# Kernel tuning notes

Measured on AMD Instinct MI355X. Metric: run time of the kernel, lower is better.

The kernel has to match this reference:

```python
import jax, jax.numpy as jnp
import numpy as np

E, K, H, I, T = 32, 4, 1024, 1024, 1024
ALPHA, BETA = 1.702, 1.0  # swiglu_alpha, swiglu_beta from the module


def setup_inputs() -> dict:
    key = jax.random.key(0)
    k0, k1, k2, k3 = jax.random.split(key, 4)
    return {
        "hidden_states": jax.random.normal(k0, (T, H), jnp.float32),
        "gate_w": jax.random.normal(k1, (H, E), jnp.float32) * (H ** -0.5),
        "gate_b": jnp.zeros((E,), jnp.float32),
        # pair_wise_act=True: gate/up are interleaved along the last dim of w1's output
        "w1": jax.random.normal(k2, (E, H, 2 * I), jnp.float32) * (H ** -0.5),
        "b1": jnp.zeros((E, 2 * I), jnp.float32),
        "w2": jax.random.normal(k3, (E, I, H), jnp.float32) * (I ** -0.5),
        "b2": jnp.zeros((E, H), jnp.float32),
    }


def reference(hidden_states, gate_w, gate_b, w1, b1, w2, b2):
    # Router gate (ReplicatedLinear with bias)
    router_logits = hidden_states @ gate_w + gate_b            # [T, E]
    probs = jax.nn.softmax(router_logits, axis=-1)
    topk_w, topk_idx = jax.lax.top_k(probs, K)                 # [T, K]
    # renormalize (norm_topk_prob=True)
    topk_w = topk_w / jnp.sum(topk_w, axis=-1, keepdims=True)
    # combine weights per (expert, token): sum over slots where idx == e
    onehot = (topk_idx[None, :, :] == jnp.arange(E)[:, None, None])  # [E, T, K]
    combine_w = jnp.sum(onehot * topk_w[None, :, :], axis=-1)        # [E, T]
    # Expert MLPs (grouped GEMM expressed as dense-per-expert einsum)
    h = jnp.einsum('th,ehd->etd', hidden_states, w1) + b1[:, None, :]  # [E, T, 2I]
    gate = h[..., 0::2]   # interleaved pairwise gate
    up = h[..., 1::2]     # interleaved pairwise up
    act = (up + BETA) * gate * jax.nn.sigmoid(ALPHA * gate)           # [E, T, I]
    y = jnp.einsum('eti,eih->eth', act, w2) + b2[:, None, :]          # [E, T, H]
    # weighted combine across selected experts
    return jnp.einsum('eth,et->th', y, combine_w)                     # [T, H]
```

## Files before the change

### kernel.cpp

```cpp
#include <hip/hip_runtime.h>
#include <hip/hip_bf16.h>
#include <math.h>

#define E_ 32
#define K_ 4
#define H_ 1024
#define I_ 1024
#define T_ 1024
#define TWO_I 2048

typedef __attribute__((ext_vector_type(4))) float float4v;
typedef __attribute__((ext_vector_type(8))) short short8v;
typedef __attribute__((ext_vector_type(4))) short short4v;

__device__ __forceinline__ unsigned short f2bf(float f) {
    unsigned u = __float_as_uint(f);
    u = (u + 0x7FFFu + ((u >> 16) & 1u)) >> 16;
    return (unsigned short)u;
}
__device__ __forceinline__ short4v cvt4(float4v v) {
    union { unsigned u[2]; short4v s; } r;
    asm("v_cvt_pk_bf16_f32 %0, %1, %2" : "=v"(r.u[0]) : "v"(v[0]), "v"(v[1]));
    asm("v_cvt_pk_bf16_f32 %0, %1, %2" : "=v"(r.u[1]) : "v"(v[2]), "v"(v[3]));
    return r.s;
}
__device__ __forceinline__ int permpos(int k4) {
    return ((k4 >> 5) << 5) + (((k4 >> 2) & 3) << 3) + (((k4 >> 4) & 1) << 2);
}

__global__ __launch_bounds__(256) void hs2bf_kernel(
    const float* __restrict__ hs, unsigned short* __restrict__ hsb) {
    int i = blockIdx.x * 256 + threadIdx.x;
    float4v v = *(const float4v*)(hs + (size_t)i * 4);
    *(short4v*)(hsb + (size_t)i * 4) = cvt4(v);
}

__global__ __launch_bounds__(256) void router_kernel(
    const float* __restrict__ hs, const float* __restrict__ gw,
    const float* __restrict__ gb, int* __restrict__ counts,
    int* __restrict__ token_list, float* __restrict__ weight_list) {
    int wv = threadIdx.x >> 6, lane = threadIdx.x & 63;
    int t = blockIdx.x * 4 + wv;
    int e = lane & 31;
    int half = lane >> 5;
    const float* hrow = hs + (size_t)t * H_;
    const float* gcol = gw + e;
    float a0 = 0.f, a1 = 0.f;
    int hb = half * 512;
#pragma unroll 4
    for (int h = 0; h < 512; h += 2) {
        a0 = fmaf(hrow[hb + h],     gcol[(size_t)(hb + h) * E_], a0);
        a1 = fmaf(hrow[hb + h + 1], gcol[(size_t)(hb + h + 1) * E_], a1);
    }
    float part = a0 + a1;
    part += __shfl_xor(part, 32);
    float cur = part + gb[e];

    int idx4[K_]; float val4[K_];
#pragma unroll
    for (int k = 0; k < K_; ++k) {
        float m = cur;
#pragma unroll
        for (int d = 1; d < 64; d <<= 1) m = fmaxf(m, __shfl_xor(m, d));
        unsigned long long b = __ballot(cur == m);
        int l = __ffsll(b) - 1;
        idx4[k] = l & 31; val4[k] = m;
        if (e == (l & 31)) cur = -INFINITY;
    }
    float mx = val4[0], s = 0.f, wv4[K_];
#pragma unroll
    for (int k = 0; k < K_; ++k) { wv4[k] = expf(val4[k] - mx); s += wv4[k]; }
    float inv = 1.f / s;
    if (lane < K_) {
        int ex = idx4[lane];
        int slot = atomicAdd(&counts[ex], 1);
        token_list[ex * T_ + slot] = t;
        weight_list[ex * T_ + slot] = wv4[lane] * inv;
    }
}

#define G_COMPUTE(BUF)                                                         \
    _Pragma("unroll")                                                          \
    for (int s = 0; s < 2; ++s) {                                              \
        short8v afr[4];                                                        \
        _Pragma("unroll")                                                      \
        for (int mi = 0; mi < 4; ++mi) {                                       \
            int row = wm * 64 + mi * 16 + l15;                                 \
            afr[mi] = *(const short8v*)&As[BUF][row * 64 + ((s * 32 + g * 8) ^ sw)]; \
        }                                                                      \
        short4v bl[2], bh[2];                                                  \
        _Pragma("unroll")                                                      \
        for (int ni = 0; ni < 2; ++ni) {                                       \
            unsigned ad = ((BUF) ? trb1 : trb0) + (unsigned)(ni * 2048 + s * 1024); \
            asm volatile("ds_read_b64_tr_b16 %0, %1" : "=v"(bl[ni]) : "v"(ad));     \
            asm volatile("ds_read_b64_tr_b16 %0, %1" : "=v"(bh[ni]) : "v"(ad + 512u)); \
        }                                                                      \
        asm volatile("s_waitcnt lgkmcnt(0)" ::: "memory");                     \
        __builtin_amdgcn_sched_barrier(0);                                     \
        _Pragma("unroll")                                                      \
        for (int ni = 0; ni < 2; ++ni) {                                       \
            short8v b;                                                         \
            b[0] = bl[ni][0]; b[1] = bl[ni][1]; b[2] = bl[ni][2]; b[3] = bl[ni][3]; \
            b[4] = bh[ni][0]; b[5] = bh[ni][1]; b[6] = bh[ni][2]; b[7] = bh[ni][3]; \
            _Pragma("unroll")                                                  \
            for (int mi = 0; mi < 4; ++mi)                                     \
                acc[mi][ni] = __builtin_amdgcn_mfma_f32_16x16x32_bf16(afr[mi], b, acc[mi][ni], 0, 0, 0); \
        }                                                                      \
    }

#define G_STEP(BUF, KN, BSTRIDE, ISLAST)                                       \
    {                                                                          \
        __syncthreads();                                                       \
        if (!(ISLAST)) {                                                       \
            _Pragma("unroll")                                                  \
            for (int i = 0; i < 4; ++i)                                        \
                ra[i] = aptr[i] ? *(const short8v*)(aptr[i] + (KN)) : z8;      \
            _Pragma("unroll")                                                  \
            for (int i = 0; i < 4; ++i)                                        \
                rb[i] = *(const float4v*)(bptrB + (size_t)(KN) * (BSTRIDE) + (size_t)(i * 16) * (BSTRIDE)); \
        }                                                                      \
        __builtin_amdgcn_sched_barrier(0);                                     \
        G_COMPUTE(BUF)                                                         \
        if (!(ISLAST)) {                                                       \
            _Pragma("unroll")                                                  \
            for (int i = 0; i < 4; ++i) {                                      \
                short8v v = ra[i];                                             \
                short4v lo, hi;                                                \
                lo[0] = v[0]; lo[1] = v[1]; lo[2] = v[2]; lo[3] = v[3];        \
                hi[0] = v[4]; hi[1] = v[5]; hi[2] = v[6]; hi[3] = v[7];        \
                *(short4v*)&As[(BUF) ^ 1][aw0[i]] = lo;                        \
                *(short4v*)&As[(BUF) ^ 1][aw1[i]] = hi;                        \
            }                                                                  \
            _Pragma("unroll")                                                  \
            for (int i = 0; i < 4; ++i) *(short4v*)&Bs[(BUF) ^ 1][bwidx[i]] = cvt4(rb[i]); \
        }                                                                      \
    }

__global__ __launch_bounds__(256, 3) void gemm1_kernel(
    const unsigned short* __restrict__ hsb, const float* __restrict__ w1,
    const float* __restrict__ b1, const int* __restrict__ counts,
    const int* __restrict__ token_list, unsigned short* __restrict__ actb) {
    int e = blockIdx.z;
    int cnt = counts[e];
    int m0 = blockIdx.y * 128;
    if (m0 >= cnt) return;
    int cb = blockIdx.x * 64;
    const float* w1e = w1 + (size_t)e * H_ * TWO_I;
    const int* tl = token_list + e * T_;

    __shared__ __align__(16) short As[2][128 * 64];
    __shared__ __align__(16) short Bs[2][64 * 64];

    int tid = threadIdx.x;
    int lane = tid & 63;
    int wid = tid >> 6;
    int wm = wid >> 1, wn = wid & 1;
    int g = lane >> 4;
    int l15 = lane & 15;
    int sw = (l15 & 7) << 3;
    unsigned trb0 = (unsigned)(size_t)(&Bs[0][0]) + (unsigned)(lane * 8) + (unsigned)(wn * 4096);
    unsigned trb1 = (unsigned)(size_t)(&Bs[1][0]) + (unsigned)(lane * 8) + (unsigned)(wn * 4096);

    int q = tid & 7;
    const unsigned short* aptr[4]; int aw0[4], aw1[4];
#pragma unroll
    for (int i = 0; i < 4; ++i) {
        int row = i * 32 + (tid >> 3);
        int gr = m0 + row;
        aptr[i] = (gr < cnt) ? hsb + (size_t)tl[gr] * H_ + q * 8 : nullptr;
        int swr = (row & 7) << 3;
        aw0[i] = row * 64 + (permpos(q * 8) ^ swr);
        aw1[i] = row * 64 + (permpos(q * 8 + 4) ^ swr);
    }
    int c4 = (tid & 15) << 2;
    const float* bptrB = w1e + (size_t)(tid >> 4) * TWO_I + cb + c4;
    int bwidx[4];
#pragma unroll
    for (int i = 0; i < 4; ++i) {
        int krow = i * 16 + (tid >> 4);
        bwidx[i] = ((c4 >> 4) * 16 + (krow >> 2)) * 64 + (krow & 3) * 16 + (c4 & 15);
    }

    float4v acc[4][2];
#pragma unroll
    for (int i = 0; i < 4; ++i)
#pragma unroll
        for (int j = 0; j < 2; ++j) acc[i][j] = (float4v){0.f, 0.f, 0.f, 0.f};

    short8v ra[4]; float4v rb[4];
    const short8v z8 = {0, 0, 0, 0, 0, 0, 0, 0};
#pragma unroll
    for (int i = 0; i < 4; ++i) ra[i] = aptr[i] ? *(const short8v*)(aptr[i]) : z8;
#pragma unroll
    for (int i = 0; i < 4; ++i) rb[i] = *(const float4v*)(bptrB + (size_t)(i * 16) * TWO_I);
#pragma unroll
    for (int i = 0; i < 4; ++i) {
        short8v v = ra[i];
        short4v lo, hi;
        lo[0] = v[0]; lo[1] = v[1]; lo[2] = v[2]; lo[3] = v[3];
        hi[0] = v[4]; hi[1] = v[5]; hi[2] = v[6]; hi[3] = v[7];
        *(short4v*)&As[0][aw0[i]] = lo;
        *(short4v*)&As[0][aw1[i]] = hi;
    }
#pragma unroll
    for (int i = 0; i < 4; ++i) *(short4v*)&Bs[0][bwidx[i]] = cvt4(rb[i]);

#pragma unroll 1
    for (int kk = 0; kk < H_; kk += 128) {
        G_STEP(0, kk + 64, TWO_I, false)
        G_STEP(1, kk + 128, TWO_I, (kk + 128) >= H_)
    }

    const float* b1e = b1 + (size_t)e * TWO_I;
#pragma unroll
    for (int mi = 0; mi < 4; ++mi) {
#pragma unroll
        for (int r = 0; r < 4; ++r) {
            int gm = m0 + wm * 64 + mi * 16 + g * 4 + r;
#pragma unroll
            for (int ni = 0; ni < 2; ++ni) {
                float v = acc[mi][ni][r];
                float o = __shfl_xor(v, 1);
                if (!(lane & 1) && gm < cnt) {
                    int wc = cb + wn * 32 + ni * 16 + l15;
                    float gate = v + b1e[wc];
                    float up   = o + b1e[wc + 1];
                    float sg = 1.f / (1.f + __expf(-1.702f * gate));
                    float av = (up + 1.f) * gate * sg;
                    actb[(size_t)(e * T_ + gm) * I_ + (wc >> 1)] = f2bf(av);
                }
            }
        }
    }
}

__global__ __launch_bounds__(256, 3) void gemm2_kernel(
    const unsigned short* __restrict__ actb, const float* __restrict__ w2,
    const float* __restrict__ b2, const int* __restrict__ counts,
    const int* __restrict__ token_list, const float* __restrict__ weight_list,
    float* __restrict__ out) {
    int e = blockIdx.z;
    int cnt = counts[e];
    int m0 = blockIdx.y * 128;
    if (m0 >= cnt) return;
    int h0 = (blockIdx.x >> 1) * 64;
    int kbase = (blockIdx.x & 1) * 512;
    const float* w2e = w2 + (size_t)e * I_ * H_;
    const int* tl = token_list + e * T_;

    __shared__ __align__(16) short As[2][128 * 64];
    __shared__ __align__(16) short Bs[2][64 * 64];

    int tid = threadIdx.x;
    int lane = tid & 63;
    int wid = tid >> 6;
    int wm = wid >> 1, wn = wid & 1;
    int g = lane >> 4;
    int l15 = lane & 15;
    int sw = (l15 & 7) << 3;
    unsigned trb0 = (unsigned)(size_t)(&Bs[0][0]) + (unsigned)(lane * 8) + (unsigned)(wn * 4096);
    unsigned trb1 = (unsigned)(size_t)(&Bs[1][0]) + (unsigned)(lane * 8) + (unsigned)(wn * 4096);

    int q = tid & 7;
    const unsigned short* aptr[4]; int aw0[4], aw1[4];
#pragma unroll
    for (int i = 0; i < 4; ++i) {
        int row = i * 32 + (tid >> 3);
        int gr = m0 + row;
        aptr[i] = (gr < cnt) ? actb + (size_t)(e * T_ + gr) * I_ + kbase + q * 8 : nullptr;
        int swr = (row & 7) << 3;
        aw0[i] = row * 64 + (permpos(q * 8) ^ swr);
        aw1[i] = row * 64 + (permpos(q * 8 + 4) ^ swr);
    }
    int c4 = (tid & 15) << 2;
    const float* bptrB = w2e + (size_t)(kbase + (tid >> 4)) * H_ + h0 + c4;
    int bwidx[4];
#pragma unroll
    for (int i = 0; i < 4; ++i) {
        int krow = i * 16 + (tid >> 4);
        bwidx[i] = ((c4 >> 4) * 16 + (krow >> 2)) * 64 + (krow & 3) * 16 + (c4 & 15);
    }

    float4v acc[4][2];
#pragma unroll
    for (int i = 0; i < 4; ++i)
#pragma unroll
        for (int j = 0; j < 2; ++j) acc[i][j] = (float4v){0.f, 0.f, 0.f, 0.f};

    short8v ra[4]; float4v rb[4];
    const short8v z8 = {0, 0, 0, 0, 0, 0, 0, 0};
#pragma unroll
    for (int i = 0; i < 4; ++i) ra[i] = aptr[i] ? *(const short8v*)(aptr[i]) : z8;
#pragma unroll
    for (int i = 0; i < 4; ++i) rb[i] = *(const float4v*)(bptrB + (size_t)(i * 16) * H_);
#pragma unroll
    for (int i = 0; i < 4; ++i) {
        short8v v = ra[i];
        short4v lo, hi;
        lo[0] = v[0]; lo[1] = v[1]; lo[2] = v[2]; lo[3] = v[3];
        hi[0] = v[4]; hi[1] = v[5]; hi[2] = v[6]; hi[3] = v[7];
        *(short4v*)&As[0][aw0[i]] = lo;
        *(short4v*)&As[0][aw1[i]] = hi;
    }
#pragma unroll
    for (int i = 0; i < 4; ++i) *(short4v*)&Bs[0][bwidx[i]] = cvt4(rb[i]);

#pragma unroll 1
    for (int kk = 0; kk < 512; kk += 128) {
        G_STEP(0, kk + 64, H_, false)
        G_STEP(1, kk + 128, H_, (kk + 128) >= 512)
    }

    const float* b2e = b2 + (size_t)e * H_;
    const float* wl = weight_list + e * T_;
    bool addbias = (kbase == 0);
#pragma unroll
    for (int mi = 0; mi < 4; ++mi) {
#pragma unroll
        for (int r = 0; r < 4; ++r) {
            int gm = m0 + wm * 64 + mi * 16 + g * 4 + r;
            if (gm < cnt) {
                int t = tl[gm];
                float wgt = wl[gm];
#pragma unroll
                for (int ni = 0; ni < 2; ++ni) {
                    int h = h0 + wn * 32 + ni * 16 + l15;
                    float v = acc[mi][ni][r];
                    if (addbias) v += b2e[h];
                    atomicAdd(&out[(size_t)t * H_ + h], v * wgt);
                }
            }
        }
    }
}

extern "C" void kernel_launch(void* const* d_in, const int* in_sizes, int n_in,
                              void* d_out, int out_size, void* d_ws, size_t ws_size,
                              hipStream_t stream) {
    const float* hs = (const float*)d_in[0];
    const float* gw = (const float*)d_in[1];
    const float* gb = (const float*)d_in[2];
    const float* w1 = (const float*)d_in[3];
    const float* b1 = (const float*)d_in[4];
    const float* w2 = (const float*)d_in[5];
    const float* b2 = (const float*)d_in[6];
    float* out = (float*)d_out;

    char* ws = (char*)d_ws;
    int*   counts      = (int*)ws;
    int*   token_list  = (int*)(ws + 4096);
    float* weight_list = (float*)(ws + 4096 + 131072);
    unsigned short* hsb  = (unsigned short*)(ws + (1 << 20));
    unsigned short* actb = (unsigned short*)(ws + (1 << 20) + (2 << 20));

    hipMemsetAsync(counts, 0, 32 * sizeof(int), stream);
    hipMemsetAsync(d_out, 0, (size_t)out_size * sizeof(float), stream);

    hs2bf_kernel<<<(T_ * H_ / 4) / 256, 256, 0, stream>>>(hs, hsb);
    router_kernel<<<T_ / 4, 256, 0, stream>>>(hs, gw, gb, counts, token_list, weight_list);
    gemm1_kernel<<<dim3(TWO_I / 64, T_ / 128, E_), 256, 0, stream>>>(
        hsb, w1, b1, counts, token_list, actb);
    gemm2_kernel<<<dim3((H_ / 64) * 2, T_ / 128, E_), 256, 0, stream>>>(
        actb, w2, b2, counts, token_list, weight_list, out);
}
```

Baseline: 203.9 us.

## Single-buffer A tile to fit four blocks per CU and fuse memsets into prep

The A operand shared-memory tile becomes single-buffered, with an extra barrier after compute before the next A tile is stored. This lowers LDS per block from 48KB to 32KB so launch bounds can rise to 4 blocks per CU. The two memsets (counts and output) move into the bf16 conversion kernel to save launches. The cost is an extra __syncthreads per k-step and less overlap between loading A and computing on it.

```diff
diff --git a/kernel.cpp b/kernel.cpp
--- a/kernel.cpp
+++ b/kernel.cpp
@@ -28,11 +28,14 @@
     return ((k4 >> 5) << 5) + (((k4 >> 2) & 3) << 3) + (((k4 >> 4) & 1) << 2);
 }
 
-__global__ __launch_bounds__(256) void hs2bf_kernel(
-    const float* __restrict__ hs, unsigned short* __restrict__ hsb) {
+__global__ __launch_bounds__(256) void prep_kernel(
+    const float* __restrict__ hs, unsigned short* __restrict__ hsb,
+    float* __restrict__ out, int* __restrict__ counts) {
     int i = blockIdx.x * 256 + threadIdx.x;
     float4v v = *(const float4v*)(hs + (size_t)i * 4);
     *(short4v*)(hsb + (size_t)i * 4) = cvt4(v);
+    *(float4v*)(out + (size_t)i * 4) = (float4v){0.f, 0.f, 0.f, 0.f};
+    if (blockIdx.x == 0 && threadIdx.x < E_) counts[threadIdx.x] = 0;
 }
 
 __global__ __launch_bounds__(256) void router_kernel(
@@ -86,7 +89,7 @@
         _Pragma("unroll")                                                      \
         for (int mi = 0; mi < 4; ++mi) {                                       \
             int row = wm * 64 + mi * 16 + l15;                                 \
-            afr[mi] = *(const short8v*)&As[BUF][row * 64 + ((s * 32 + g * 8) ^ sw)]; \
+            afr[mi] = *(const short8v*)&As[row * 64 + ((s * 32 + g * 8) ^ sw)]; \
         }                                                                      \
         short4v bl[2], bh[2];                                                  \
         _Pragma("unroll")                                                      \
@@ -121,6 +124,7 @@
         }                                                                      \
         __builtin_amdgcn_sched_barrier(0);                                     \
         G_COMPUTE(BUF)                                                         \
+        __syncthreads();                                                       \
         if (!(ISLAST)) {                                                       \
             _Pragma("unroll")                                                  \
             for (int i = 0; i < 4; ++i) {                                      \
@@ -128,15 +132,15 @@
                 short4v lo, hi;                                                \
                 lo[0] = v[0]; lo[1] = v[1]; lo[2] = v[2]; lo[3] = v[3];        \
                 hi[0] = v[4]; hi[1] = v[5]; hi[2] = v[6]; hi[3] = v[7];        \
-                *(short4v*)&As[(BUF) ^ 1][aw0[i]] = lo;                        \
-                *(short4v*)&As[(BUF) ^ 1][aw1[i]] = hi;                        \
+                *(short4v*)&As[aw0[i]] = lo;                                   \
+                *(short4v*)&As[aw1[i]] = hi;                                   \
             }                                                                  \
             _Pragma("unroll")                                                  \
             for (int i = 0; i < 4; ++i) *(short4v*)&Bs[(BUF) ^ 1][bwidx[i]] = cvt4(rb[i]); \
         }                                                                      \
     }
 
-__global__ __launch_bounds__(256, 3) void gemm1_kernel(
+__global__ __launch_bounds__(256, 4) void gemm1_kernel(
     const unsigned short* __restrict__ hsb, const float* __restrict__ w1,
     const float* __restrict__ b1, const int* __restrict__ counts,
     const int* __restrict__ token_list, unsigned short* __restrict__ actb) {
@@ -148,7 +152,7 @@
     const float* w1e = w1 + (size_t)e * H_ * TWO_I;
     const int* tl = token_list + e * T_;
 
-    __shared__ __align__(16) short As[2][128 * 64];
+    __shared__ __align__(16) short As[128 * 64];
     __shared__ __align__(16) short Bs[2][64 * 64];
 
     int tid = threadIdx.x;
@@ -199,8 +203,8 @@
         short4v lo, hi;
         lo[0] = v[0]; lo[1] = v[1]; lo[2] = v[2]; lo[3] = v[3];
         hi[0] = v[4]; hi[1] = v[5]; hi[2] = v[6]; hi[3] = v[7];
-        *(short4v*)&As[0][aw0[i]] = lo;
-        *(short4v*)&As[0][aw1[i]] = hi;
+        *(short4v*)&As[aw0[i]] = lo;
+        *(short4v*)&As[aw1[i]] = hi;
     }
 #pragma unroll
     for (int i = 0; i < 4; ++i) *(short4v*)&Bs[0][bwidx[i]] = cvt4(rb[i]);
@@ -234,7 +238,7 @@
     }
 }
 
-__global__ __launch_bounds__(256, 3) void gemm2_kernel(
+__global__ __launch_bounds__(256, 4) void gemm2_kernel(
     const unsigned short* __restrict__ actb, const float* __restrict__ w2,
     const float* __restrict__ b2, const int* __restrict__ counts,
     const int* __restrict__ token_list, const float* __restrict__ weight_list,
@@ -248,7 +252,7 @@
     const float* w2e = w2 + (size_t)e * I_ * H_;
     const int* tl = token_list + e * T_;
 
-    __shared__ __align__(16) short As[2][128 * 64];
+    __shared__ __align__(16) short As[128 * 64];
     __shared__ __align__(16) short Bs[2][64 * 64];
 
     int tid = threadIdx.x;
@@ -299,8 +303,8 @@
         short4v lo, hi;
         lo[0] = v[0]; lo[1] = v[1]; lo[2] = v[2]; lo[3] = v[3];
         hi[0] = v[4]; hi[1] = v[5]; hi[2] = v[6]; hi[3] = v[7];
-        *(short4v*)&As[0][aw0[i]] = lo;
-        *(short4v*)&As[0][aw1[i]] = hi;
+        *(short4v*)&As[aw0[i]] = lo;
+        *(short4v*)&As[aw1[i]] = hi;
     }
 #pragma unroll
     for (int i = 0; i < 4; ++i) *(short4v*)&Bs[0][bwidx[i]] = cvt4(rb[i]);
@@ -353,10 +357,7 @@
     unsigned short* hsb  = (unsigned short*)(ws + (1 << 20));
     unsigned short* actb = (unsigned short*)(ws + (1 << 20) + (2 << 20));
 
-    hipMemsetAsync(counts, 0, 32 * sizeof(int), stream);
-    hipMemsetAsync(d_out, 0, (size_t)out_size * sizeof(float), stream);
-
-    hs2bf_kernel<<<(T_ * H_ / 4) / 256, 256, 0, stream>>>(hs, hsb);
+    prep_kernel<<<(T_ * H_ / 4) / 256, 256, 0, stream>>>(hs, hsb, out, counts);
     router_kernel<<<T_ / 4, 256, 0, stream>>>(hs, gw, gb, counts, token_list, weight_list);
     gemm1_kernel<<<dim3(TWO_I / 64, T_ / 128, E_), 256, 0, stream>>>(
         hsb, w1, b1, counts, token_list, actb);
```

After: 271.6 us. 33.2% more time.
